# Optimization experiments

Hardware: AMD Instinct MI355X
Metric: run time of the kernel (lower is better)

## Reference

```python
import jax, jax.numpy as jnp
import numpy as np

N, E, IN_DIM, OUT_DIM, EDGE_DIM = 50000, 800000, 256, 128, 64
NEG_SLOPE = 0.2


def setup_inputs() -> dict:
    key = jax.random.key(0)
    ks = jax.random.split(key, 8)
    xavier = lambda k, shape: jax.random.normal(k, shape, jnp.float32) * np.float32(np.sqrt(2.0 / (shape[0] + shape[1])))
    return {
        "nfeat": jax.random.normal(ks[0], (N, IN_DIM), jnp.float32),
        "ex": jax.random.normal(ks[1], (E, EDGE_DIM), jnp.float32),
        "src": jax.random.randint(ks[2], (E,), 0, N),
        "dst": jax.random.randint(ks[3], (E,), 0, N),
        "W_fc": xavier(ks[4], (OUT_DIM, IN_DIM)),
        "b_fc": jnp.zeros((OUT_DIM,), jnp.float32),
        "W_att": xavier(ks[5], (1, 2 * OUT_DIM + EDGE_DIM)),
        "b_att": jnp.zeros((1,), jnp.float32),
        "W_edge": xavier(ks[6], (OUT_DIM, EDGE_DIM)),
        "b_edge": jnp.zeros((OUT_DIM,), jnp.float32),
        "W_eatt": xavier(ks[7], (EDGE_DIM, EDGE_DIM)),
        "b_eatt": jnp.zeros((EDGE_DIM,), jnp.float32),
    }


def reference(nfeat, ex, src, dst, W_fc, b_fc, W_att, b_att, W_edge, b_edge, W_eatt, b_eatt):
    n = nfeat.shape[0]
    # node transform: z = fc(nfeat)  [N, OUT]
    z = nfeat @ W_fc.T + b_fc
    # edge transform for attention score calc  [E, EDGE_DIM]
    ex_t = ex @ W_eatt.T + b_eatt
    z_src = z[src]                                   # [E, OUT] gather
    # attention logits on concat[z_src, z_dst, ex_t]  [E, 1]
    z2 = jnp.concatenate([z_src, z[dst], ex_t], axis=1)
    e = jax.nn.leaky_relu(z2 @ W_att.T + b_att, NEG_SLOPE)
    # edge feature message  [E, OUT]
    ez = ex @ W_edge.T + b_edge
    # segment softmax over incoming edges of each dst node
    m = jax.ops.segment_max(e, dst, num_segments=n)  # [N, 1]
    w = jnp.exp(e - m[dst])
    denom = jax.ops.segment_sum(w, dst, num_segments=n)
    alpha = w / denom[dst]                           # [E, 1]
    # h = sum_e alpha * z_src + sum_e alpha * ez (apply_attention_on_edge)
    h = jax.ops.segment_sum(alpha * (z_src + ez), dst, num_segments=n)  # [N, OUT]
    return h, alpha
```

## Files before the change

### kernel.cpp

```cpp
#include <hip/hip_runtime.h>
#include <math.h>
#include <float.h>

#define IN_D 256
#define OUT_D 128
#define ED_D 64
#define NEG 0.2f

typedef __attribute__((ext_vector_type(8))) short bf16x8;
typedef __attribute__((ext_vector_type(4))) float f32x4;

__device__ __forceinline__ unsigned short f2bf(float f) {
    unsigned u = __float_as_uint(f);
    unsigned r = (u + 0x7FFFu + ((u >> 16) & 1u)) >> 16;
    return (unsigned short)r;
}

__global__ __launch_bounds__(256) void k_init(
        const float* __restrict__ W_att, const float* __restrict__ b_att,
        const float* __restrict__ W_eatt, const float* __restrict__ b_eatt,
        const float* __restrict__ W_fc, const float* __restrict__ W_edge,
        float* __restrict__ u, float* __restrict__ c0,
        unsigned short* __restrict__ Wb, float2* __restrict__ Wt2,
        int* __restrict__ cnt, int N) {
    int idx = blockIdx.x * 256 + threadIdx.x;
    if (idx < N) cnt[idx] = 0;
    if (idx < IN_D * OUT_D) {
        int i = idx & 7;
        int lane = (idx >> 3) & 63;
        int rest = idx >> 9;
        int nt = rest & 7, ks = rest >> 3;
        int col = nt * 16 + (lane & 15);
        int k = ks * 32 + (lane >> 4) * 8 + i;
        Wb[idx] = f2bf(W_fc[col * IN_D + k]);
    }
    if (idx < ED_D * (OUT_D / 2)) {
        int k = idx >> 6, l = idx & 63;
        Wt2[idx] = make_float2(W_edge[(2 * l) * ED_D + k], W_edge[(2 * l + 1) * ED_D + k]);
    }
    if (idx < ED_D) {
        float acc = 0.f;
        for (int j = 0; j < ED_D; ++j) acc += W_att[256 + j] * W_eatt[j * ED_D + idx];
        u[idx] = acc;
    }
    if (idx == ED_D) {
        float c = 0.f;
        for (int j = 0; j < ED_D; ++j) c += W_att[256 + j] * b_eatt[j];
        c0[0] = c + b_att[0];
    }
}

__global__ __launch_bounds__(256) void k_hist(const int* __restrict__ dst,
                                              int* __restrict__ cnt,
                                              int* __restrict__ rank, int E) {
    int i = blockIdx.x * 256 + threadIdx.x;
    if (i < E) rank[i] = atomicAdd(&cnt[dst[i]], 1);
}

#define LDA 272
__global__ __launch_bounds__(256) void k_node(
        const float* __restrict__ nfeat, const unsigned short* __restrict__ Wb,
        const float* __restrict__ b_fc, const float* __restrict__ W_att,
        float* __restrict__ z, float* __restrict__ asrc, float* __restrict__ adst, int n) {
    __shared__ unsigned short sa[128 * LDA];
    int t = threadIdx.x;
    int row_base = blockIdx.x * 128;

    int r8 = t >> 3, c8 = t & 7;
#pragma unroll
    for (int p = 0; p < 4; ++p) {
        int r = p * 32 + r8;
        int node = row_base + r; if (node >= n) node = n - 1;
        const float4* srcp = (const float4*)(nfeat + (size_t)node * IN_D);
#pragma unroll
        for (int q = 0; q < 8; ++q) {
            int c4 = q * 8 + c8;
            float4 v = srcp[c4];
            unsigned pk0 = (unsigned)f2bf(v.x) | ((unsigned)f2bf(v.y) << 16);
            unsigned pk1 = (unsigned)f2bf(v.z) | ((unsigned)f2bf(v.w) << 16);
            *(uint2*)&sa[(size_t)r * LDA + c4 * 4] = make_uint2(pk0, pk1);
        }
    }
    __syncthreads();

    int lane = t & 63, w = t >> 6;
    int lr = lane & 15, lg = lane >> 4;

    f32x4 acc[2][8];
#pragma unroll
    for (int mi = 0; mi < 2; ++mi)
#pragma unroll
        for (int nt = 0; nt < 8; ++nt) acc[mi][nt] = (f32x4)(0.f);

    const bf16x8* wb8 = (const bf16x8*)Wb;
#pragma unroll
    for (int ks = 0; ks < 8; ++ks) {
        bf16x8 af[2], bfr[8];
#pragma unroll
        for (int mi = 0; mi < 2; ++mi) {
            int row = (2 * w + mi) * 16 + lr;
            af[mi] = *(const bf16x8*)&sa[(size_t)row * LDA + ks * 32 + lg * 8];
        }
#pragma unroll
        for (int nt = 0; nt < 8; ++nt)
            bfr[nt] = wb8[(ks * 8 + nt) * 64 + lane];
#pragma unroll
        for (int mi = 0; mi < 2; ++mi)
#pragma unroll
            for (int nt = 0; nt < 8; ++nt)
                acc[mi][nt] = __builtin_amdgcn_mfma_f32_16x16x32_bf16(
                    af[mi], bfr[nt], acc[mi][nt], 0, 0, 0);
    }

    float w1c[8], w2c[8], bfc[8];
#pragma unroll
    for (int nt = 0; nt < 8; ++nt) {
        int col = nt * 16 + lr;
        w1c[nt] = W_att[col];
        w2c[nt] = W_att[128 + col];
        bfc[nt] = b_fc[col];
    }
#pragma unroll
    for (int mi = 0; mi < 2; ++mi) {
        float p1[4] = {0.f, 0.f, 0.f, 0.f}, p2[4] = {0.f, 0.f, 0.f, 0.f};
#pragma unroll
        for (int nt = 0; nt < 8; ++nt) {
#pragma unroll
            for (int reg = 0; reg < 4; ++reg) {
                float zv = acc[mi][nt][reg] + bfc[nt];
                int m = row_base + (2 * w + mi) * 16 + lg * 4 + reg;
                if (m < n) z[(size_t)m * OUT_D + nt * 16 + lr] = zv;
                p1[reg] = fmaf(zv, w1c[nt], p1[reg]);
                p2[reg] = fmaf(zv, w2c[nt], p2[reg]);
            }
        }
#pragma unroll
        for (int reg = 0; reg < 4; ++reg) {
#pragma unroll
            for (int off = 1; off <= 8; off <<= 1) {
                p1[reg] += __shfl_xor(p1[reg], off);
                p2[reg] += __shfl_xor(p2[reg], off);
            }
        }
        if (lr == 0) {
#pragma unroll
            for (int reg = 0; reg < 4; ++reg) {
                int m = row_base + (2 * w + mi) * 16 + lg * 4 + reg;
                if (m < n) { asrc[m] = p1[reg]; adst[m] = p2[reg]; }
            }
        }
    }
}

__global__ __launch_bounds__(1024) void k_scan(const int* __restrict__ cnt,
                                               int* __restrict__ rowptr, int N) {
    int t = threadIdx.x;
    int per = (N + 1023) / 1024;
    int b0 = t * per, b1 = b0 + per;
    if (b0 > N) b0 = N;
    if (b1 > N) b1 = N;
    int s = 0;
    for (int i = b0; i < b1; ++i) s += cnt[i];
    int wl = t & 63, w = t >> 6;
    int v = s;
#pragma unroll
    for (int off = 1; off < 64; off <<= 1) {
        int a = __shfl_up(v, off);
        if (wl >= off) v += a;
    }
    __shared__ int wsum[16], woff[16];
    if (wl == 63) wsum[w] = v;
    __syncthreads();
    if (t == 0) { int r = 0; for (int i = 0; i < 16; ++i) { woff[i] = r; r += wsum[i]; } }
    __syncthreads();
    int run = woff[w] + v - s;
    for (int i = b0; i < b1; ++i) { rowptr[i] = run; run += cnt[i]; }
    if (t == 1023) rowptr[N] = run;
}

__global__ __launch_bounds__(256) void k_edge(
        const float* __restrict__ ex, const int* __restrict__ src, const int* __restrict__ dst,
        const float* __restrict__ asrc, const float* __restrict__ adst,
        const float* __restrict__ u, const float* __restrict__ c0,
        const int* __restrict__ rowptr, const int* __restrict__ rank,
        int2* __restrict__ csr, int E) {
    int i = blockIdx.x * 256 + threadIdx.x;
    if (i >= E) return;
    const float4* exr = (const float4*)(ex + (size_t)i * ED_D);
    const float4* u4 = (const float4*)u;
    float acc = 0.f;
#pragma unroll
    for (int q = 0; q < 16; ++q) {
        float4 a = exr[q], b = u4[q];
        acc += a.x * b.x + a.y * b.y + a.z * b.z + a.w * b.w;
    }
    int s = src[i], d = dst[i];
    float e = acc + asrc[s] + adst[d] + c0[0];
    e = (e > 0.f) ? e : NEG * e;
    int pos = rowptr[d] + rank[i];
    csr[pos] = make_int2(__float_as_int(e), i);
}

__global__ __launch_bounds__(256) void k_gather(
        const float4* __restrict__ zf4, const float2* __restrict__ ex2,
        const int* __restrict__ srcv, const int2* __restrict__ csr,
        const int* __restrict__ rowptr,
        float4* __restrict__ h4, float* __restrict__ alpha_out,
        float2* __restrict__ xsum2, int N) {
    int lane = threadIdx.x & 63;
    int half = lane >> 5, hl = lane & 31;
    int n = blockIdx.x * 4 + (threadIdx.x >> 6);
    if (n >= N) return;
    int beg = rowptr[n], end = rowptr[n + 1];
    int deg = end - beg;
    if (deg == 0) return;
    float4 accz = make_float4(0.f, 0.f, 0.f, 0.f);
    float2 accx = make_float2(0.f, 0.f);

    if (deg <= 64) {
        int2 me = make_int2(0, 0);
        int sl = 0;
        float lg = -FLT_MAX;
        if (lane < deg) {
            me = csr[beg + lane];
            lg = __int_as_float(me.x);
            sl = srcv[me.y];
        }
        float m = lg;
#pragma unroll
        for (int off = 32; off >= 1; off >>= 1) m = fmaxf(m, __shfl_xor(m, off));
        float wvv = (lane < deg) ? expf(lg - m) : 0.f;
        float sw = wvv;
#pragma unroll
        for (int off = 32; off >= 1; off >>= 1) sw += __shfl_xor(sw, off);
        float al = wvv / sw;
        if (lane < deg) alpha_out[me.y] = al;
        int j = 0;
        for (; j + 8 <= deg; j += 8) {
            float a[4]; int s[4], e[4];
#pragma unroll
            for (int q = 0; q < 4; ++q) {
                int idx = j + 2 * q + half;
                a[q] = __shfl(al, idx);
                s[q] = __shfl(sl, idx);
                e[q] = __shfl(me.y, idx);
            }
            float4 zv[4]; float2 xv[4];
#pragma unroll
            for (int q = 0; q < 4; ++q) {
                zv[q] = zf4[(size_t)s[q] * 32 + hl];
                xv[q] = ex2[(size_t)e[q] * 32 + hl];
            }
#pragma unroll
            for (int q = 0; q < 4; ++q) {
                accz.x = fmaf(a[q], zv[q].x, accz.x);
                accz.y = fmaf(a[q], zv[q].y, accz.y);
                accz.z = fmaf(a[q], zv[q].z, accz.z);
                accz.w = fmaf(a[q], zv[q].w, accz.w);
                accx.x = fmaf(a[q], xv[q].x, accx.x);
                accx.y = fmaf(a[q], xv[q].y, accx.y);
            }
        }
        if (j + 4 <= deg) {
            float a[2]; int s[2], e[2];
#pragma unroll
            for (int q = 0; q < 2; ++q) {
                int idx = j + 2 * q + half;
                a[q] = __shfl(al, idx);
                s[q] = __shfl(sl, idx);
                e[q] = __shfl(me.y, idx);
            }
            float4 zv[2]; float2 xv[2];
#pragma unroll
            for (int q = 0; q < 2; ++q) {
                zv[q] = zf4[(size_t)s[q] * 32 + hl];
                xv[q] = ex2[(size_t)e[q] * 32 + hl];
            }
#pragma unroll
            for (int q = 0; q < 2; ++q) {
                accz.x = fmaf(a[q], zv[q].x, accz.x);
                accz.y = fmaf(a[q], zv[q].y, accz.y);
                accz.z = fmaf(a[q], zv[q].z, accz.z);
                accz.w = fmaf(a[q], zv[q].w, accz.w);
                accx.x = fmaf(a[q], xv[q].x, accx.x);
                accx.y = fmaf(a[q], xv[q].y, accx.y);
            }
            j += 4;
        }
        for (; j < deg; j += 2) {
            int idx = j + half;
            float a = __shfl(al, idx);
            int s = __shfl(sl, idx), e = __shfl(me.y, idx);
            float4 zv = zf4[(size_t)s * 32 + hl];
            float2 xv = ex2[(size_t)e * 32 + hl];
            accz.x = fmaf(a, zv.x, accz.x);
            accz.y = fmaf(a, zv.y, accz.y);
            accz.z = fmaf(a, zv.z, accz.z);
            accz.w = fmaf(a, zv.w, accz.w);
            accx.x = fmaf(a, xv.x, accx.x);
            accx.y = fmaf(a, xv.y, accx.y);
        }
    } else {
        float m = -FLT_MAX;
        for (int c = beg + lane; c < end; c += 64)
            m = fmaxf(m, __int_as_float(csr[c].x));
#pragma unroll
        for (int off = 32; off >= 1; off >>= 1) m = fmaxf(m, __shfl_xor(m, off));
        float sw = 0.f;
        for (int c = beg + lane; c < end; c += 64)
            sw += expf(__int_as_float(csr[c].x) - m);
#pragma unroll
        for (int off = 32; off >= 1; off >>= 1) sw += __shfl_xor(sw, off);
        float rden = 1.f / sw;
        for (int c = beg; c < end; c += 64) {
            int mcnt = end - c;
            if (mcnt > 64) mcnt = 64;
            int2 me = make_int2(0, 0);
            int sl = 0;
            float al = 0.f;
            if (lane < mcnt) {
                me = csr[c + lane];
                al = expf(__int_as_float(me.x) - m) * rden;
                alpha_out[me.y] = al;
                sl = srcv[me.y];
            }
            int j = 0;
            for (; j + 8 <= mcnt; j += 8) {
                float a[4]; int s[4], e[4];
#pragma unroll
                for (int q = 0; q < 4; ++q) {
                    int idx = j + 2 * q + half;
                    a[q] = __shfl(al, idx);
                    s[q] = __shfl(sl, idx);
                    e[q] = __shfl(me.y, idx);
                }
                float4 zv[4]; float2 xv[4];
#pragma unroll
                for (int q = 0; q < 4; ++q) {
                    zv[q] = zf4[(size_t)s[q] * 32 + hl];
                    xv[q] = ex2[(size_t)e[q] * 32 + hl];
                }
#pragma unroll
                for (int q = 0; q < 4; ++q) {
                    accz.x = fmaf(a[q], zv[q].x, accz.x);
                    accz.y = fmaf(a[q], zv[q].y, accz.y);
                    accz.z = fmaf(a[q], zv[q].z, accz.z);
                    accz.w = fmaf(a[q], zv[q].w, accz.w);
                    accx.x = fmaf(a[q], xv[q].x, accx.x);
                    accx.y = fmaf(a[q], xv[q].y, accx.y);
                }
            }
            for (; j < mcnt; j += 2) {
                int idx = j + half;
                float a = __shfl(al, idx);
                int s = __shfl(sl, idx), e = __shfl(me.y, idx);
                float4 zv = zf4[(size_t)s * 32 + hl];
                float2 xv = ex2[(size_t)e * 32 + hl];
                accz.x = fmaf(a, zv.x, accz.x);
                accz.y = fmaf(a, zv.y, accz.y);
                accz.z = fmaf(a, zv.z, accz.z);
                accz.w = fmaf(a, zv.w, accz.w);
                accx.x = fmaf(a, xv.x, accx.x);
                accx.y = fmaf(a, xv.y, accx.y);
            }
        }
    }
    accz.x += __shfl_xor(accz.x, 32);
    accz.y += __shfl_xor(accz.y, 32);
    accz.z += __shfl_xor(accz.z, 32);
    accz.w += __shfl_xor(accz.w, 32);
    accx.x += __shfl_xor(accx.x, 32);
    accx.y += __shfl_xor(accx.y, 32);
    if (half == 0) {
        h4[(size_t)n * 32 + hl] = accz;
        xsum2[(size_t)n * 32 + hl] = accx;
    }
}

__global__ __launch_bounds__(256) void k_xmm(
        const float2* __restrict__ Wt2, const float* __restrict__ b_edge,
        const float* __restrict__ xsum, const int* __restrict__ rowptr,
        float2* __restrict__ h2, int N) {
    __shared__ float2 swt[ED_D * 64];
    for (int i = threadIdx.x; i < ED_D * 64; i += 256) swt[i] = Wt2[i];
    __syncthreads();
    int lane = threadIdx.x & 63;
    int wv = threadIdx.x >> 6;
    float2 be2 = ((const float2*)b_edge)[lane];
    for (int n = blockIdx.x * 4 + wv; n < N; n += gridDim.x * 4) {
        int deg = rowptr[n + 1] - rowptr[n];
        if (deg == 0) {
            h2[(size_t)n * 64 + lane] = make_float2(0.f, 0.f);
            continue;
        }
        float xk = xsum[(size_t)n * 64 + lane];
        float2 hv = h2[(size_t)n * 64 + lane];
        hv.x += be2.x; hv.y += be2.y;
#pragma unroll 8
        for (int k = 0; k < 64; ++k) {
            float a = __shfl(xk, k);
            float2 w2 = swt[k * 64 + lane];
            hv.x = fmaf(a, w2.x, hv.x);
            hv.y = fmaf(a, w2.y, hv.y);
        }
        h2[(size_t)n * 64 + lane] = hv;
    }
}

extern "C" void kernel_launch(void* const* d_in, const int* in_sizes, int n_in,
                              void* d_out, int out_size, void* d_ws, size_t ws_size,
                              hipStream_t stream) {
    const float* nfeat = (const float*)d_in[0];
    const float* ex    = (const float*)d_in[1];
    const int*   src   = (const int*)d_in[2];
    const int*   dst   = (const int*)d_in[3];
    const float* W_fc  = (const float*)d_in[4];
    const float* b_fc  = (const float*)d_in[5];
    const float* W_att = (const float*)d_in[6];
    const float* b_att = (const float*)d_in[7];
    const float* W_edge = (const float*)d_in[8];
    const float* b_edge = (const float*)d_in[9];
    const float* W_eatt = (const float*)d_in[10];
    const float* b_eatt = (const float*)d_in[11];
    int N = in_sizes[0] / IN_D;
    int E = in_sizes[2];

    float* h_out = (float*)d_out;
    float* alpha_out = h_out + (size_t)N * OUT_D;

    char* w = (char*)d_ws;
    auto alloc = [&](size_t bytes) { char* p = w; w += (bytes + 255) & ~255ull; return p; };
    float* z      = (float*)alloc((size_t)N * OUT_D * 4);
    float* asrc   = (float*)alloc((size_t)N * 4);
    float* adst   = (float*)alloc((size_t)N * 4);
    int* cnt      = (int*)alloc((size_t)N * 4);
    int* rowptr   = (int*)alloc(((size_t)N + 1) * 4);
    int* rank     = (int*)alloc((size_t)E * 4);
    int2* csr     = (int2*)alloc((size_t)E * 8);
    float* xsum   = (float*)alloc((size_t)N * ED_D * 4);
    unsigned short* Wb = (unsigned short*)alloc((size_t)IN_D * OUT_D * 2);
    float2* Wt2   = (float2*)alloc((size_t)ED_D * 64 * 8);
    float* u      = (float*)alloc(64 * 4);
    float* c0     = (float*)alloc(4);

    int init_total = N > IN_D * OUT_D ? N : IN_D * OUT_D;
    k_init<<<(init_total + 255) / 256, 256, 0, stream>>>(
        W_att, b_att, W_eatt, b_eatt, W_fc, W_edge, u, c0, Wb, Wt2, cnt, N);
    k_hist<<<(E + 255) / 256, 256, 0, stream>>>(dst, cnt, rank, E);
    k_node<<<(N + 127) / 128, 256, 0, stream>>>(nfeat, Wb, b_fc, W_att, z, asrc, adst, N);
    k_scan<<<1, 1024, 0, stream>>>(cnt, rowptr, N);
    k_edge<<<(E + 255) / 256, 256, 0, stream>>>(ex, src, dst, asrc, adst, u, c0,
                                                rowptr, rank, csr, E);
    k_gather<<<(N + 3) / 4, 256, 0, stream>>>((const float4*)z, (const float2*)ex, src, csr,
                                              rowptr, (float4*)h_out, alpha_out,
                                              (float2*)xsum, N);
    k_xmm<<<(N + 3) / 4, 256, 0, stream>>>((const float2*)Wt2, b_edge, xsum, rowptr,
                                           (float2*)h_out, N);
}
```

Measured before the change: 411.2 us.

## Fuse edge logit computation into per-node gather to read ex once

Replaces the per-edge logit kernel and the gather kernel with a lightweight CSR fill (edge id and src) and a fused per-node kernel. The fused kernel loads each incoming edge's ex row once and uses it both for the attention logit (wave-reduced dot with u) and for the weighted ex sum. This removes the second full pass over the 200MB ex tensor and the separate csr logit writes. In exchange it adds a 6-step shuffle reduction per edge, a 32-entry register array (register pressure), and a serial online-softmax path for nodes with degree above 32.

```diff
diff --git a/kernel.cpp b/kernel.cpp
--- a/kernel.cpp
+++ b/kernel.cpp
@@ -178,202 +178,177 @@
     if (t == 1023) rowptr[N] = run;
 }
 
-__global__ __launch_bounds__(256) void k_edge(
-        const float* __restrict__ ex, const int* __restrict__ src, const int* __restrict__ dst,
+__global__ __launch_bounds__(256) void k_fill(
+        const int* __restrict__ dst, const int* __restrict__ src,
+        const int* __restrict__ rank, const int* __restrict__ rowptr,
+        int* __restrict__ eid_csr, int* __restrict__ src_csr, int E) {
+    int i = blockIdx.x * 256 + threadIdx.x;
+    if (i >= E) return;
+    int d = dst[i];
+    int pos = rowptr[d] + rank[i];
+    eid_csr[pos] = i;
+    src_csr[pos] = src[i];
+}
+
+__global__ __launch_bounds__(256) void k_fused(
+        const float* __restrict__ z, const float* __restrict__ ex,
+        const int* __restrict__ eid_csr, const int* __restrict__ src_csr,
+        const int* __restrict__ rowptr,
         const float* __restrict__ asrc, const float* __restrict__ adst,
         const float* __restrict__ u, const float* __restrict__ c0,
-        const int* __restrict__ rowptr, const int* __restrict__ rank,
-        int2* __restrict__ csr, int E) {
-    int i = blockIdx.x * 256 + threadIdx.x;
-    if (i >= E) return;
-    const float4* exr = (const float4*)(ex + (size_t)i * ED_D);
-    const float4* u4 = (const float4*)u;
-    float acc = 0.f;
-#pragma unroll
-    for (int q = 0; q < 16; ++q) {
-        float4 a = exr[q], b = u4[q];
-        acc += a.x * b.x + a.y * b.y + a.z * b.z + a.w * b.w;
-    }
-    int s = src[i], d = dst[i];
-    float e = acc + asrc[s] + adst[d] + c0[0];
-    e = (e > 0.f) ? e : NEG * e;
-    int pos = rowptr[d] + rank[i];
-    csr[pos] = make_int2(__float_as_int(e), i);
-}
-
-__global__ __launch_bounds__(256) void k_gather(
-        const float4* __restrict__ zf4, const float2* __restrict__ ex2,
-        const int* __restrict__ srcv, const int2* __restrict__ csr,
-        const int* __restrict__ rowptr,
-        float4* __restrict__ h4, float* __restrict__ alpha_out,
-        float2* __restrict__ xsum2, int N) {
+        float* __restrict__ h, float* __restrict__ alpha_out,
+        float* __restrict__ xsum, int N) {
     int lane = threadIdx.x & 63;
-    int half = lane >> 5, hl = lane & 31;
     int n = blockIdx.x * 4 + (threadIdx.x >> 6);
     if (n >= N) return;
     int beg = rowptr[n], end = rowptr[n + 1];
     int deg = end - beg;
     if (deg == 0) return;
-    float4 accz = make_float4(0.f, 0.f, 0.f, 0.f);
-    float2 accx = make_float2(0.f, 0.f);
-
-    if (deg <= 64) {
-        int2 me = make_int2(0, 0);
-        int sl = 0;
+    float uv = u[lane];
+    float adn = adst[n];
+    float cc = c0[0];
+
+    if (deg <= 32) {
+        int e = 0, s = 0;
         float lg = -FLT_MAX;
         if (lane < deg) {
-            me = csr[beg + lane];
-            lg = __int_as_float(me.x);
-            sl = srcv[me.y];
+            e = eid_csr[beg + lane];
+            s = src_csr[beg + lane];
+        }
+        float v[32];
+#pragma unroll
+        for (int j = 0; j < 32; ++j) {
+            float val = 0.f;
+            if (j < deg) {
+                int ej = __shfl(e, j);
+                val = ex[(size_t)ej * ED_D + lane];
+                float p = val * uv;
+#pragma unroll
+                for (int off = 32; off >= 1; off >>= 1) p += __shfl_xor(p, off);
+                if (lane == j) lg = p;
+            }
+            v[j] = val;
+        }
+        if (lane < deg) {
+            lg += asrc[s] + adn + cc;
+            lg = (lg > 0.f) ? lg : NEG * lg;
+        } else {
+            lg = -FLT_MAX;
         }
         float m = lg;
 #pragma unroll
         for (int off = 32; off >= 1; off >>= 1) m = fmaxf(m, __shfl_xor(m, off));
-        float wvv = (lane < deg) ? expf(lg - m) : 0.f;
-        float sw = wvv;
+        float wv = (lane < deg) ? expf(lg - m) : 0.f;
+        float sw = wv;
 #pragma unroll
         for (int off = 32; off >= 1; off >>= 1) sw += __shfl_xor(sw, off);
-        float al = wvv / sw;
-        if (lane < deg) alpha_out[me.y] = al;
+        float al = wv / sw;
+        if (lane < deg) alpha_out[e] = al;
+
+        float accxs = 0.f;
+#pragma unroll
+        for (int j = 0; j < 32; ++j) {
+            if (j < deg) {
+                float a = __shfl(al, j);
+                accxs = fmaf(a, v[j], accxs);
+            }
+        }
+
+        int half = lane >> 5, hl = lane & 31;
+        const float4* zf4 = (const float4*)z;
+        float4 accz = make_float4(0.f, 0.f, 0.f, 0.f);
         int j = 0;
         for (; j + 8 <= deg; j += 8) {
-            float a[4]; int s[4], e[4];
+            float a[4]; int sv[4];
 #pragma unroll
             for (int q = 0; q < 4; ++q) {
                 int idx = j + 2 * q + half;
                 a[q] = __shfl(al, idx);
-                s[q] = __shfl(sl, idx);
-                e[q] = __shfl(me.y, idx);
-            }
-            float4 zv[4]; float2 xv[4];
-#pragma unroll
-            for (int q = 0; q < 4; ++q) {
-                zv[q] = zf4[(size_t)s[q] * 32 + hl];
-                xv[q] = ex2[(size_t)e[q] * 32 + hl];
-            }
+                sv[q] = __shfl(s, idx);
+            }
+            float4 zv[4];
+#pragma unroll
+            for (int q = 0; q < 4; ++q) zv[q] = zf4[(size_t)sv[q] * 32 + hl];
 #pragma unroll
             for (int q = 0; q < 4; ++q) {
                 accz.x = fmaf(a[q], zv[q].x, accz.x);
                 accz.y = fmaf(a[q], zv[q].y, accz.y);
                 accz.z = fmaf(a[q], zv[q].z, accz.z);
                 accz.w = fmaf(a[q], zv[q].w, accz.w);
-                accx.x = fmaf(a[q], xv[q].x, accx.x);
-                accx.y = fmaf(a[q], xv[q].y, accx.y);
             }
         }
         if (j + 4 <= deg) {
-            float a[2]; int s[2], e[2];
+            float a[2]; int sv[2];
 #pragma unroll
             for (int q = 0; q < 2; ++q) {
                 int idx = j + 2 * q + half;
                 a[q] = __shfl(al, idx);
-                s[q] = __shfl(sl, idx);
-                e[q] = __shfl(me.y, idx);
-            }
-            float4 zv[2]; float2 xv[2];
-#pragma unroll
-            for (int q = 0; q < 2; ++q) {
-                zv[q] = zf4[(size_t)s[q] * 32 + hl];
-                xv[q] = ex2[(size_t)e[q] * 32 + hl];
-            }
+                sv[q] = __shfl(s, idx);
+            }
+            float4 zv[2];
+#pragma unroll
+            for (int q = 0; q < 2; ++q) zv[q] = zf4[(size_t)sv[q] * 32 + hl];
 #pragma unroll
             for (int q = 0; q < 2; ++q) {
                 accz.x = fmaf(a[q], zv[q].x, accz.x);
                 accz.y = fmaf(a[q], zv[q].y, accz.y);
                 accz.z = fmaf(a[q], zv[q].z, accz.z);
                 accz.w = fmaf(a[q], zv[q].w, accz.w);
-                accx.x = fmaf(a[q], xv[q].x, accx.x);
-                accx.y = fmaf(a[q], xv[q].y, accx.y);
             }
             j += 4;
         }
         for (; j < deg; j += 2) {
             int idx = j + half;
             float a = __shfl(al, idx);
-            int s = __shfl(sl, idx), e = __shfl(me.y, idx);
-            float4 zv = zf4[(size_t)s * 32 + hl];
-            float2 xv = ex2[(size_t)e * 32 + hl];
+            int sv = __shfl(s, idx);
+            float4 zv = zf4[(size_t)sv * 32 + hl];
             accz.x = fmaf(a, zv.x, accz.x);
             accz.y = fmaf(a, zv.y, accz.y);
             accz.z = fmaf(a, zv.z, accz.z);
             accz.w = fmaf(a, zv.w, accz.w);
-            accx.x = fmaf(a, xv.x, accx.x);
-            accx.y = fmaf(a, xv.y, accx.y);
-        }
+        }
+        accz.x += __shfl_xor(accz.x, 32);
+        accz.y += __shfl_xor(accz.y, 32);
+        accz.z += __shfl_xor(accz.z, 32);
+        accz.w += __shfl_xor(accz.w, 32);
+        if (half == 0) ((float4*)h)[(size_t)n * 32 + hl] = accz;
+        xsum[(size_t)n * ED_D + lane] = accxs;
     } else {
-        float m = -FLT_MAX;
-        for (int c = beg + lane; c < end; c += 64)
-            m = fmaxf(m, __int_as_float(csr[c].x));
-#pragma unroll
-        for (int off = 32; off >= 1; off >>= 1) m = fmaxf(m, __shfl_xor(m, off));
-        float sw = 0.f;
-        for (int c = beg + lane; c < end; c += 64)
-            sw += expf(__int_as_float(csr[c].x) - m);
-#pragma unroll
-        for (int off = 32; off >= 1; off >>= 1) sw += __shfl_xor(sw, off);
-        float rden = 1.f / sw;
-        for (int c = beg; c < end; c += 64) {
-            int mcnt = end - c;
-            if (mcnt > 64) mcnt = 64;
-            int2 me = make_int2(0, 0);
-            int sl = 0;
-            float al = 0.f;
-            if (lane < mcnt) {
-                me = csr[c + lane];
-                al = expf(__int_as_float(me.x) - m) * rden;
-                alpha_out[me.y] = al;
-                sl = srcv[me.y];
-            }
-            int j = 0;
-            for (; j + 8 <= mcnt; j += 8) {
-                float a[4]; int s[4], e[4];
-#pragma unroll
-                for (int q = 0; q < 4; ++q) {
-                    int idx = j + 2 * q + half;
-                    a[q] = __shfl(al, idx);
-                    s[q] = __shfl(sl, idx);
-                    e[q] = __shfl(me.y, idx);
-                }
-                float4 zv[4]; float2 xv[4];
-#pragma unroll
-                for (int q = 0; q < 4; ++q) {
-                    zv[q] = zf4[(size_t)s[q] * 32 + hl];
-                    xv[q] = ex2[(size_t)e[q] * 32 + hl];
-                }
-#pragma unroll
-                for (int q = 0; q < 4; ++q) {
-                    accz.x = fmaf(a[q], zv[q].x, accz.x);
-                    accz.y = fmaf(a[q], zv[q].y, accz.y);
-                    accz.z = fmaf(a[q], zv[q].z, accz.z);
-                    accz.w = fmaf(a[q], zv[q].w, accz.w);
-                    accx.x = fmaf(a[q], xv[q].x, accx.x);
-                    accx.y = fmaf(a[q], xv[q].y, accx.y);
-                }
-            }
-            for (; j < mcnt; j += 2) {
-                int idx = j + half;
-                float a = __shfl(al, idx);
-                int s = __shfl(sl, idx), e = __shfl(me.y, idx);
-                float4 zv = zf4[(size_t)s * 32 + hl];
-                float2 xv = ex2[(size_t)e * 32 + hl];
-                accz.x = fmaf(a, zv.x, accz.x);
-                accz.y = fmaf(a, zv.y, accz.y);
-                accz.z = fmaf(a, zv.z, accz.z);
-                accz.w = fmaf(a, zv.w, accz.w);
-                accx.x = fmaf(a, xv.x, accx.x);
-                accx.y = fmaf(a, xv.y, accx.y);
-            }
-        }
-    }
-    accz.x += __shfl_xor(accz.x, 32);
-    accz.y += __shfl_xor(accz.y, 32);
-    accz.z += __shfl_xor(accz.z, 32);
-    accz.w += __shfl_xor(accz.w, 32);
-    accx.x += __shfl_xor(accx.x, 32);
-    accx.y += __shfl_xor(accx.y, 32);
-    if (half == 0) {
-        h4[(size_t)n * 32 + hl] = accz;
-        xsum2[(size_t)n * 32 + hl] = accx;
+        float m = -FLT_MAX, ssum = 0.f;
+        for (int i = beg; i < end; ++i) {
+            int e = eid_csr[i];
+            float xv = ex[(size_t)e * ED_D + lane];
+            float p = xv * uv;
+#pragma unroll
+            for (int off = 32; off >= 1; off >>= 1) p += __shfl_xor(p, off);
+            float lg = p + asrc[src_csr[i]] + adn + cc;
+            lg = (lg > 0.f) ? lg : NEG * lg;
+            float mn = fmaxf(m, lg);
+            ssum = ssum * expf(m - mn) + expf(lg - mn);
+            m = mn;
+        }
+        float rden = 1.f / ssum;
+        const float2* z2 = (const float2*)z;
+        float2 accz2 = make_float2(0.f, 0.f);
+        float accxs = 0.f;
+        for (int i = beg; i < end; ++i) {
+            int e = eid_csr[i];
+            int s = src_csr[i];
+            float xv = ex[(size_t)e * ED_D + lane];
+            float p = xv * uv;
+#pragma unroll
+            for (int off = 32; off >= 1; off >>= 1) p += __shfl_xor(p, off);
+            float lg = p + asrc[s] + adn + cc;
+            lg = (lg > 0.f) ? lg : NEG * lg;
+            float al = expf(lg - m) * rden;
+            if (lane == 0) alpha_out[e] = al;
+            accxs = fmaf(al, xv, accxs);
+            float2 zv = z2[(size_t)s * ED_D + lane];
+            accz2.x = fmaf(al, zv.x, accz2.x);
+            accz2.y = fmaf(al, zv.y, accz2.y);
+        }
+        ((float2*)h)[(size_t)n * ED_D + lane] = accz2;
+        xsum[(size_t)n * ED_D + lane] = accxs;
     }
 }
 
@@ -436,7 +411,8 @@
     int* cnt      = (int*)alloc((size_t)N * 4);
     int* rowptr   = (int*)alloc(((size_t)N + 1) * 4);
     int* rank     = (int*)alloc((size_t)E * 4);
-    int2* csr     = (int2*)alloc((size_t)E * 8);
+    int* eid_csr  = (int*)alloc((size_t)E * 4);
+    int* src_csr  = (int*)alloc((size_t)E * 4);
     float* xsum   = (float*)alloc((size_t)N * ED_D * 4);
     unsigned short* Wb = (unsigned short*)alloc((size_t)IN_D * OUT_D * 2);
     float2* Wt2   = (float2*)alloc((size_t)ED_D * 64 * 8);
@@ -449,11 +425,9 @@
     k_hist<<<(E + 255) / 256, 256, 0, stream>>>(dst, cnt, rank, E);
     k_node<<<(N + 127) / 128, 256, 0, stream>>>(nfeat, Wb, b_fc, W_att, z, asrc, adst, N);
     k_scan<<<1, 1024, 0, stream>>>(cnt, rowptr, N);
-    k_edge<<<(E + 255) / 256, 256, 0, stream>>>(ex, src, dst, asrc, adst, u, c0,
-                                                rowptr, rank, csr, E);
-    k_gather<<<(N + 3) / 4, 256, 0, stream>>>((const float4*)z, (const float2*)ex, src, csr,
-                                              rowptr, (float4*)h_out, alpha_out,
-                                              (float2*)xsum, N);
+    k_fill<<<(E + 255) / 256, 256, 0, stream>>>(dst, src, rank, rowptr, eid_csr, src_csr, E);
+    k_fused<<<(N + 3) / 4, 256, 0, stream>>>(z, ex, eid_csr, src_csr, rowptr, asrc, adst,
+                                             u, c0, h_out, alpha_out, xsum, N);
     k_xmm<<<(N + 3) / 4, 256, 0, stream>>>((const float2*)Wt2, b_edge, xsum, rowptr,
                                            (float2*)h_out, N);
 }
```

After: 429.3 us. +4.4%, slower.
